# Kernel tuning notes

Measured on AMD Instinct MI355X. Metric: run time of the kernel, lower is better.

The kernel has to match this reference:

```python
import jax, jax.numpy as jnp
import numpy as np

TAU = 2.0
V_TH = 0.5
SG_ALPHA = 4.0
BN_EPS = 1e-5
NUM_HEADS = 8

@jax.custom_vjp
def spike_fn(x):
    return (x >= 0.0).astype(x.dtype)

def _spike_fwd(x):
    return (x >= 0.0).astype(x.dtype), x

def _spike_bwd(x, g):
    s = jax.nn.sigmoid(SG_ALPHA * x)
    return (g * SG_ALPHA * s * (1.0 - s),)

spike_fn.defvjp(_spike_fwd, _spike_bwd)

def lif(x_seq):
    """Multi-step LIF (spikingjelly step_mode='m'): x_seq [T, ...] -> spikes [T, ...].
    v <- v + (x - v)/tau ; spike = H(v - v_th) ; hard reset with detached spike."""
    def step(v, x):
        v = v + (x - v) / TAU
        s = spike_fn(v - V_TH)
        v = v * (1.0 - jax.lax.stop_gradient(s))
        return v, s
    _, s_seq = jax.lax.scan(step, jnp.zeros_like(x_seq[0]), x_seq)
    return s_seq

def conv1x1(x, w, b=None):
    # x: [T,B,C,H,W], w: [Cout,Cin]
    y = jnp.einsum('tbchw,oc->tbohw', x, w)
    if b is not None:
        y = y + b[:, None, None]
    return y

def bn(x, p):
    # eval-mode BatchNorm2d; p = [gamma, beta, mean, var] each [C]
    g, b, m, v = p[0], p[1], p[2], p[3]
    scale = g / jnp.sqrt(v + BN_EPS)
    return x * scale[:, None, None] + (b - m * scale)[:, None, None]

def setup_inputs() -> dict:
    key = jax.random.key(0)
    ks = jax.random.split(key, 20)
    T, B, C, H, W = 4, 8, 512, 32, 32
    Ch = 2048
    def bn_params(k, c):
        kk = jax.random.split(k, 4)
        gamma = jax.random.uniform(kk[0], (c,), jnp.float32, 0.5, 1.5)
        beta = jax.random.normal(kk[1], (c,), jnp.float32) * 0.1
        mean = jax.random.normal(kk[2], (c,), jnp.float32) * 0.1
        var = jax.random.uniform(kk[3], (c,), jnp.float32, 0.5, 1.5)
        return jnp.stack([gamma, beta, mean, var])
    s = 1.0 / np.sqrt(C)
    sh = 1.0 / np.sqrt(Ch)
    return {
        'x': jax.random.normal(ks[0], (T, B, C, H, W), jnp.float32),
        'q_w': jax.random.normal(ks[1], (C, C), jnp.float32) * s,
        'q_bn': bn_params(ks[2], C),
        'k_w': jax.random.normal(ks[3], (C, C), jnp.float32) * s,
        'k_bn': bn_params(ks[4], C),
        'v_w': jax.random.normal(ks[5], (C, C), jnp.float32) * s,
        'v_bn': bn_params(ks[6], C),
        'th_w': jax.random.normal(ks[7], (NUM_HEADS, NUM_HEADS), jnp.float32) / np.sqrt(NUM_HEADS),
        'proj_w': jax.random.normal(ks[8], (C, C), jnp.float32) * s,
        'proj_b': jax.random.normal(ks[9], (C,), jnp.float32) * 0.02,
        'proj_bn': bn_params(ks[10], C),
        'fc1_w': jax.random.normal(ks[11], (Ch, C), jnp.float32) * s,
        'fc1_b': jax.random.normal(ks[12], (Ch,), jnp.float32) * 0.02,
        'fc1_bn': bn_params(ks[13], Ch),
        'fc2_w': jax.random.normal(ks[14], (C, Ch), jnp.float32) * sh,
        'fc2_b': jax.random.normal(ks[15], (C,), jnp.float32) * 0.02,
        'fc2_bn': bn_params(ks[16], C),
    }

def reference(x, q_w, q_bn, k_w, k_bn, v_w, v_bn, th_w, proj_w, proj_b, proj_bn,
              fc1_w, fc1_b, fc1_bn, fc2_w, fc2_b, fc2_bn):
    T, B, C, H, W = x.shape
    N = H * W
    h = NUM_HEADS
    d = C // h

    # ---- MS_SSA_Conv ----
    identity = x
    xs = lif(x)  # shortcut_lif

    def to_heads(t):  # [T,B,C,H,W] -> [T,B,h,N,d]
        t = t.reshape(T, B, C, N).transpose(0, 1, 3, 2)        # [T,B,N,C]
        return t.reshape(T, B, N, h, d).transpose(0, 1, 3, 2, 4)

    q = to_heads(lif(bn(conv1x1(xs, q_w), q_bn)))
    k = to_heads(lif(bn(conv1x1(xs, k_w), k_bn)))
    v = to_heads(lif(bn(conv1x1(xs, v_w), v_bn)))

    kv = (k * v).sum(axis=3, keepdims=True)                    # [T,B,h,1,d]
    kv = jnp.einsum('tbhod,gh->tbgod', kv, th_w)               # talking heads (Conv1d k=1)
    kv = lif(kv)                                               # talking_heads_lif

    x_att = q * kv                                             # [T,B,h,N,d]
    x_att = x_att.transpose(0, 1, 2, 4, 3).reshape(T, B, C, H, W)
    x_out = bn(conv1x1(x_att, proj_w, proj_b), proj_bn) + identity

    # ---- MS_MLP_Conv (res=False since hidden != in) ----
    identity2 = x_out
    hdn = lif(bn(conv1x1(x_out, fc1_w, fc1_b), fc1_bn))
    out = lif(bn(conv1x1(hdn, fc2_w, fc2_b), fc2_bn)) + identity2
    return out
```

## Files before the change

### kernel.cpp

```cpp
#include <hip/hip_runtime.h>

typedef unsigned char u8;
typedef unsigned int u32;

#define T_STEPS 4
#define B_SZ 8
#define C_IN 512
#define CH 2048
#define N_SP 1024
#define S_C ((size_t)B_SZ * C_IN * N_SP)

__global__ __launch_bounds__(256) void lif_x_kernel(const float* __restrict__ in,
                                                    u8* __restrict__ out)
{
    size_t i = (size_t)blockIdx.x * 256 + threadIdx.x;
    float v = 0.0f;
    #pragma unroll
    for (int t = 0; t < T_STEPS; ++t) {
        float x = in[(size_t)t * S_C + i];
        v += (x - v) * 0.5f;
        u8 s = (v >= 0.5f) ? 1 : 0;
        out[(size_t)t * S_C + i] = s;
        v = s ? 0.0f : v;
    }
}

template<int MODE, int BSRC, bool BIAS, int K, int CO, int NSEL>
__global__ __launch_bounds__(256) void mm(
    const float* __restrict__ W0, const float* __restrict__ W1, const float* __restrict__ W2,
    const void* __restrict__ Xv,
    const float* __restrict__ bn0, const float* __restrict__ bn1, const float* __restrict__ bn2,
    const float* __restrict__ bias,
    const float* __restrict__ kvsf,
    const float* __restrict__ res,
    void* Y0, void* Y1, void* Y2)
{
    constexpr int BM = 64;
    constexpr int NB_CO = CO / BM;
    constexpr int KT = K / 16;

    __shared__ float As[16][72];
    __shared__ float Xs[16][136];

    const int bid = blockIdx.x;
    const int nblk = bid & 7;
    int slot = bid >> 3;
    const int cb = slot % NB_CO; slot /= NB_CO;
    const int sel = (NSEL > 1) ? (slot % NSEL) : 0;
    const int b   = (NSEL > 1) ? (slot / NSEL) : slot;

    const float* W   = (NSEL == 1 || sel == 0) ? W0  : (sel == 1 ? W1  : W2);
    const float* bnp = (NSEL == 1 || sel == 0) ? bn0 : (sel == 1 ? bn1 : bn2);
    void* Yv         = (NSEL == 1 || sel == 0) ? Y0  : (sel == 1 ? Y1  : Y2);

    const int coBase = cb * BM;
    const int n0blk = nblk * 128;
    const int tid = threadIdx.x;
    const int tx = tid & 15, ty = tid >> 4;

    const int wr = tid >> 2;
    const int wk4 = (tid & 3) * 4;

    float scale[4], shift[4];
    #pragma unroll
    for (int i = 0; i < 4; ++i) {
        const int co = coBase + ty * 4 + i;
        const float g = bnp[co], be = bnp[CO + co];
        const float mn = bnp[2 * CO + co], vr = bnp[3 * CO + co];
        scale[i] = g / sqrtf(vr + 1e-5f);
        shift[i] = be - mn * scale[i];
        if (BIAS) shift[i] += bias[co] * scale[i];
    }

    float vst[4][8];
    if (MODE != 1) {
        #pragma unroll
        for (int i = 0; i < 4; ++i)
            #pragma unroll
            for (int j = 0; j < 8; ++j) vst[i][j] = 0.0f;
    }

    for (int t = 0; t < T_STEPS; ++t) {
        const int tb = t * B_SZ + b;
        const u8* Xu = (const u8*)Xv + (size_t)tb * K * N_SP;
        const float* Xf = (const float*)Xv + (size_t)tb * K * N_SP;

        float acc[4][8];
        #pragma unroll
        for (int i = 0; i < 4; ++i)
            #pragma unroll
            for (int j = 0; j < 8; ++j) acc[i][j] = 0.0f;

        float4 wreg;
        u32 xa, xb;
        float mreg = 1.0f;
        float4 xfa, xfb;

        auto prefetch = [&](int kt) {
            wreg = *reinterpret_cast<const float4*>(
                W + (size_t)(coBase + wr) * K + kt * 16 + wk4);
            if constexpr (BSRC <= 1) {
                const u8* xp = Xu + (size_t)(kt * 16 + ty) * N_SP + n0blk + tx * 4;
                xa = *reinterpret_cast<const u32*>(xp);
                xb = *reinterpret_cast<const u32*>(xp + 64);
                if constexpr (BSRC == 1)
                    mreg = kvsf[(size_t)tb * K + kt * 16 + ty];
            } else {
                const float* xp = Xf + (size_t)(kt * 16 + ty) * N_SP + n0blk + tx * 4;
                xfa = *reinterpret_cast<const float4*>(xp);
                xfb = *reinterpret_cast<const float4*>(xp + 64);
            }
        };

        prefetch(0);

        for (int kt = 0; kt < KT; ++kt) {
            __syncthreads();
            As[wk4 + 0][wr] = wreg.x;
            As[wk4 + 1][wr] = wreg.y;
            As[wk4 + 2][wr] = wreg.z;
            As[wk4 + 3][wr] = wreg.w;
            if constexpr (BSRC <= 1) {
                float4 s0, s1;
                s0.x = (float)( xa        & 0xFFu);
                s0.y = (float)((xa >> 8 ) & 0xFFu);
                s0.z = (float)((xa >> 16) & 0xFFu);
                s0.w = (float)( xa >> 24        );
                s1.x = (float)( xb        & 0xFFu);
                s1.y = (float)((xb >> 8 ) & 0xFFu);
                s1.z = (float)((xb >> 16) & 0xFFu);
                s1.w = (float)( xb >> 24        );
                if constexpr (BSRC == 1) {
                    s0.x *= mreg; s0.y *= mreg; s0.z *= mreg; s0.w *= mreg;
                    s1.x *= mreg; s1.y *= mreg; s1.z *= mreg; s1.w *= mreg;
                }
                *reinterpret_cast<float4*>(&Xs[ty][tx * 4]) = s0;
                *reinterpret_cast<float4*>(&Xs[ty][tx * 4 + 64]) = s1;
            } else {
                *reinterpret_cast<float4*>(&Xs[ty][tx * 4]) = xfa;
                *reinterpret_cast<float4*>(&Xs[ty][tx * 4 + 64]) = xfb;
            }
            __syncthreads();
            if (kt + 1 < KT) prefetch(kt + 1);

            #pragma unroll
            for (int kk = 0; kk < 16; ++kk) {
                float4 av = *reinterpret_cast<const float4*>(&As[kk][ty * 4]);
                float4 x0 = *reinterpret_cast<const float4*>(&Xs[kk][tx * 4]);
                float4 x1 = *reinterpret_cast<const float4*>(&Xs[kk][tx * 4 + 64]);
                float wa[4] = {av.x, av.y, av.z, av.w};
                float xw[8] = {x0.x, x0.y, x0.z, x0.w, x1.x, x1.y, x1.z, x1.w};
                #pragma unroll
                for (int i = 0; i < 4; ++i)
                    #pragma unroll
                    for (int j = 0; j < 8; ++j)
                        acc[i][j] += wa[i] * xw[j];
            }
        }

        #pragma unroll
        for (int i = 0; i < 4; ++i) {
            const int co = coBase + ty * 4 + i;
            const size_t base = ((size_t)tb * CO + co) * N_SP + n0blk + tx * 4;
            if constexpr (MODE == 0) {
                u32 p0 = 0, p1 = 0;
                #pragma unroll
                for (int j = 0; j < 8; ++j) {
                    const float y = acc[i][j] * scale[i] + shift[i];
                    float v = vst[i][j];
                    v += (y - v) * 0.5f;
                    const u32 s = (v >= 0.5f) ? 1u : 0u;
                    vst[i][j] = s ? 0.0f : v;
                    if (j < 4) p0 |= s << (8 * j); else p1 |= s << (8 * (j - 4));
                }
                *reinterpret_cast<u32*>((u8*)Yv + base) = p0;
                *reinterpret_cast<u32*>((u8*)Yv + base + 64) = p1;
            } else if constexpr (MODE == 1) {
                float4 r0 = *reinterpret_cast<const float4*>(res + base);
                float4 r1 = *reinterpret_cast<const float4*>(res + base + 64);
                float rr[8] = {r0.x, r0.y, r0.z, r0.w, r1.x, r1.y, r1.z, r1.w};
                float o[8];
                #pragma unroll
                for (int j = 0; j < 8; ++j)
                    o[j] = acc[i][j] * scale[i] + shift[i] + rr[j];
                float4 s0 = {o[0], o[1], o[2], o[3]};
                float4 s1 = {o[4], o[5], o[6], o[7]};
                *reinterpret_cast<float4*>((float*)Yv + base) = s0;
                *reinterpret_cast<float4*>((float*)Yv + base + 64) = s1;
            } else {
                float* op = (float*)Yv + base;
                float4 r0 = *reinterpret_cast<const float4*>(op);
                float4 r1 = *reinterpret_cast<const float4*>(op + 64);
                float rr[8] = {r0.x, r0.y, r0.z, r0.w, r1.x, r1.y, r1.z, r1.w};
                float o[8];
                #pragma unroll
                for (int j = 0; j < 8; ++j) {
                    const float y = acc[i][j] * scale[i] + shift[i];
                    float v = vst[i][j];
                    v += (y - v) * 0.5f;
                    const u32 s = (v >= 0.5f) ? 1u : 0u;
                    vst[i][j] = s ? 0.0f : v;
                    o[j] = rr[j] + (s ? 1.0f : 0.0f);
                }
                float4 s0 = {o[0], o[1], o[2], o[3]};
                float4 s1 = {o[4], o[5], o[6], o[7]};
                *reinterpret_cast<float4*>(op) = s0;
                *reinterpret_cast<float4*>(op + 64) = s1;
            }
        }
    }
}

__global__ __launch_bounds__(256) void kv_reduce(const u8* __restrict__ ks,
                                                 const u8* __restrict__ vs,
                                                 float* __restrict__ kv)
{
    const int row = blockIdx.x * 4 + (threadIdx.x >> 6);
    const int lane = threadIdx.x & 63;
    const u8* kp = ks + (size_t)row * N_SP;
    const u8* vp = vs + (size_t)row * N_SP;
    int acc = 0;
    #pragma unroll
    for (int n = 0; n < N_SP; n += 256) {
        uchar4 a = *reinterpret_cast<const uchar4*>(kp + n + lane * 4);
        uchar4 c = *reinterpret_cast<const uchar4*>(vp + n + lane * 4);
        acc += (a.x & c.x) + (a.y & c.y) + (a.z & c.z) + (a.w & c.w);
    }
    #pragma unroll
    for (int off = 32; off; off >>= 1) acc += __shfl_down(acc, off, 64);
    if (lane == 0) kv[row] = (float)acc;
}

__global__ __launch_bounds__(256) void th_lif(const float* __restrict__ kvraw,
                                              const float* __restrict__ th,
                                              float* __restrict__ kvs)
{
    const int i = blockIdx.x * 256 + threadIdx.x;
    const int b = i >> 9;
    const int c = i & 511;
    const int g = c >> 6;
    const int dd = c & 63;
    float v = 0.0f;
    #pragma unroll
    for (int t = 0; t < T_STEPS; ++t) {
        const float* base = kvraw + ((size_t)t * B_SZ + b) * C_IN;
        float x = 0.0f;
        #pragma unroll
        for (int hh = 0; hh < 8; ++hh)
            x += base[hh * 64 + dd] * th[g * 8 + hh];
        v += (x - v) * 0.5f;
        const float s = (v >= 0.5f) ? 1.0f : 0.0f;
        kvs[((size_t)t * B_SZ + b) * C_IN + c] = s;
        v = (s != 0.0f) ? 0.0f : v;
    }
}

extern "C" void kernel_launch(void* const* d_in, const int* in_sizes, int n_in,
                              void* d_out, int out_size, void* d_ws, size_t ws_size,
                              hipStream_t stream)
{
    const float* x       = (const float*)d_in[0];
    const float* q_w     = (const float*)d_in[1];
    const float* q_bn    = (const float*)d_in[2];
    const float* k_w     = (const float*)d_in[3];
    const float* k_bn    = (const float*)d_in[4];
    const float* v_w     = (const float*)d_in[5];
    const float* v_bn    = (const float*)d_in[6];
    const float* th_w    = (const float*)d_in[7];
    const float* proj_w  = (const float*)d_in[8];
    const float* proj_b  = (const float*)d_in[9];
    const float* proj_bn = (const float*)d_in[10];
    const float* fc1_w   = (const float*)d_in[11];
    const float* fc1_b   = (const float*)d_in[12];
    const float* fc1_bn  = (const float*)d_in[13];
    const float* fc2_w   = (const float*)d_in[14];
    const float* fc2_b   = (const float*)d_in[15];
    const float* fc2_bn  = (const float*)d_in[16];
    float* out = (float*)d_out;

    u8* ws = (u8*)d_ws;
    const size_t SLOT = (size_t)T_STEPS * S_C;
    u8* xs = ws;
    u8* qs = ws + SLOT;
    u8* ks = ws + 2 * SLOT;
    u8* vs = ws + 3 * SLOT;
    float* kvraw = (float*)(ws + 4 * SLOT);
    float* kvsf  = kvraw + (size_t)T_STEPS * B_SZ * C_IN;
    u8* hdn = ws;

    lif_x_kernel<<<(int)(S_C / 256), 256, 0, stream>>>(x, xs);

    mm<0, 0, false, 512, 512, 3><<<1536, 256, 0, stream>>>(
        q_w, k_w, v_w, xs, q_bn, k_bn, v_bn, nullptr, nullptr, nullptr, qs, ks, vs);

    kv_reduce<<<(T_STEPS * B_SZ * C_IN) / 4, 256, 0, stream>>>(ks, vs, kvraw);
    th_lif<<<(B_SZ * C_IN) / 256, 256, 0, stream>>>(kvraw, th_w, kvsf);

    mm<1, 1, true, 512, 512, 1><<<512, 256, 0, stream>>>(
        proj_w, nullptr, nullptr, qs, proj_bn, nullptr, nullptr, proj_b, kvsf, x,
        out, nullptr, nullptr);

    mm<0, 2, true, 512, 2048, 1><<<2048, 256, 0, stream>>>(
        fc1_w, nullptr, nullptr, out, fc1_bn, nullptr, nullptr, fc1_b, nullptr, nullptr,
        hdn, nullptr, nullptr);

    mm<2, 0, true, 2048, 512, 1><<<512, 256, 0, stream>>>(
        fc2_w, nullptr, nullptr, hdn, fc2_bn, nullptr, nullptr, fc2_b, nullptr, nullptr,
        out, nullptr, nullptr);
}
```

Measured before the change: 2.641 ms.

## Double-buffer LDS tiles in the fused GEMM and prefetch across timesteps

Shared-memory tiles are now double-buffered, so each k-step needs one barrier instead of two. The next tile is staged into the alternate buffer after the compute, and prefetching carries across timestep boundaries so the pipeline does not drain at each t. This doubles LDS usage and changes the As row padding, which may affect occupancy and bank conflicts.

```diff
diff --git a/kernel.cpp b/kernel.cpp
--- a/kernel.cpp
+++ b/kernel.cpp
@@ -39,8 +39,8 @@
     constexpr int NB_CO = CO / BM;
     constexpr int KT = K / 16;
 
-    __shared__ float As[16][72];
-    __shared__ float Xs[16][136];
+    __shared__ float As[2][16][76];
+    __shared__ float Xs[2][16][136];
 
     const int bid = blockIdx.x;
     const int nblk = bid & 7;
@@ -80,10 +80,63 @@
             for (int j = 0; j < 8; ++j) vst[i][j] = 0.0f;
     }
 
+    float4 wreg;
+    u32 xa, xb;
+    float mreg = 1.0f;
+    float4 xfa, xfb;
+
+    auto prefetch = [&](int tbq, int kt) {
+        wreg = *reinterpret_cast<const float4*>(
+            W + (size_t)(coBase + wr) * K + kt * 16 + wk4);
+        if constexpr (BSRC <= 1) {
+            const u8* xp = (const u8*)Xv + (size_t)tbq * K * N_SP
+                           + (size_t)(kt * 16 + ty) * N_SP + n0blk + tx * 4;
+            xa = *reinterpret_cast<const u32*>(xp);
+            xb = *reinterpret_cast<const u32*>(xp + 64);
+            if constexpr (BSRC == 1)
+                mreg = kvsf[(size_t)tbq * K + kt * 16 + ty];
+        } else {
+            const float* xp = (const float*)Xv + (size_t)tbq * K * N_SP
+                              + (size_t)(kt * 16 + ty) * N_SP + n0blk + tx * 4;
+            xfa = *reinterpret_cast<const float4*>(xp);
+            xfb = *reinterpret_cast<const float4*>(xp + 64);
+        }
+    };
+
+    auto stage = [&](int pp) {
+        As[pp][wk4 + 0][wr] = wreg.x;
+        As[pp][wk4 + 1][wr] = wreg.y;
+        As[pp][wk4 + 2][wr] = wreg.z;
+        As[pp][wk4 + 3][wr] = wreg.w;
+        if constexpr (BSRC <= 1) {
+            float4 s0, s1;
+            s0.x = (float)( xa        & 0xFFu);
+            s0.y = (float)((xa >> 8 ) & 0xFFu);
+            s0.z = (float)((xa >> 16) & 0xFFu);
+            s0.w = (float)( xa >> 24        );
+            s1.x = (float)( xb        & 0xFFu);
+            s1.y = (float)((xb >> 8 ) & 0xFFu);
+            s1.z = (float)((xb >> 16) & 0xFFu);
+            s1.w = (float)( xb >> 24        );
+            if constexpr (BSRC == 1) {
+                s0.x *= mreg; s0.y *= mreg; s0.z *= mreg; s0.w *= mreg;
+                s1.x *= mreg; s1.y *= mreg; s1.z *= mreg; s1.w *= mreg;
+            }
+            *reinterpret_cast<float4*>(&Xs[pp][ty][tx * 4]) = s0;
+            *reinterpret_cast<float4*>(&Xs[pp][ty][tx * 4 + 64]) = s1;
+        } else {
+            *reinterpret_cast<float4*>(&Xs[pp][ty][tx * 4]) = xfa;
+            *reinterpret_cast<float4*>(&Xs[pp][ty][tx * 4 + 64]) = xfb;
+        }
+    };
+
+    int p = 0;
+    prefetch(b, 0);
+    stage(0);
+    __syncthreads();
+
     for (int t = 0; t < T_STEPS; ++t) {
         const int tb = t * B_SZ + b;
-        const u8* Xu = (const u8*)Xv + (size_t)tb * K * N_SP;
-        const float* Xf = (const float*)Xv + (size_t)tb * K * N_SP;
 
         float acc[4][8];
         #pragma unroll
@@ -91,63 +144,18 @@
             #pragma unroll
             for (int j = 0; j < 8; ++j) acc[i][j] = 0.0f;
 
-        float4 wreg;
-        u32 xa, xb;
-        float mreg = 1.0f;
-        float4 xfa, xfb;
-
-        auto prefetch = [&](int kt) {
-            wreg = *reinterpret_cast<const float4*>(
-                W + (size_t)(coBase + wr) * K + kt * 16 + wk4);
-            if constexpr (BSRC <= 1) {
-                const u8* xp = Xu + (size_t)(kt * 16 + ty) * N_SP + n0blk + tx * 4;
-                xa = *reinterpret_cast<const u32*>(xp);
-                xb = *reinterpret_cast<const u32*>(xp + 64);
-                if constexpr (BSRC == 1)
-                    mreg = kvsf[(size_t)tb * K + kt * 16 + ty];
-            } else {
-                const float* xp = Xf + (size_t)(kt * 16 + ty) * N_SP + n0blk + tx * 4;
-                xfa = *reinterpret_cast<const float4*>(xp);
-                xfb = *reinterpret_cast<const float4*>(xp + 64);
-            }
-        };
-
-        prefetch(0);
-
         for (int kt = 0; kt < KT; ++kt) {
-            __syncthreads();
-            As[wk4 + 0][wr] = wreg.x;
-            As[wk4 + 1][wr] = wreg.y;
-            As[wk4 + 2][wr] = wreg.z;
-            As[wk4 + 3][wr] = wreg.w;
-            if constexpr (BSRC <= 1) {
-                float4 s0, s1;
-                s0.x = (float)( xa        & 0xFFu);
-                s0.y = (float)((xa >> 8 ) & 0xFFu);
-                s0.z = (float)((xa >> 16) & 0xFFu);
-                s0.w = (float)( xa >> 24        );
-                s1.x = (float)( xb        & 0xFFu);
-                s1.y = (float)((xb >> 8 ) & 0xFFu);
-                s1.z = (float)((xb >> 16) & 0xFFu);
-                s1.w = (float)( xb >> 24        );
-                if constexpr (BSRC == 1) {
-                    s0.x *= mreg; s0.y *= mreg; s0.z *= mreg; s0.w *= mreg;
-                    s1.x *= mreg; s1.y *= mreg; s1.z *= mreg; s1.w *= mreg;
-                }
-                *reinterpret_cast<float4*>(&Xs[ty][tx * 4]) = s0;
-                *reinterpret_cast<float4*>(&Xs[ty][tx * 4 + 64]) = s1;
-            } else {
-                *reinterpret_cast<float4*>(&Xs[ty][tx * 4]) = xfa;
-                *reinterpret_cast<float4*>(&Xs[ty][tx * 4 + 64]) = xfb;
-            }
-            __syncthreads();
-            if (kt + 1 < KT) prefetch(kt + 1);
-
+            const bool last = (kt == KT - 1) && (t == T_STEPS - 1);
+            if (!last) {
+                const int nkt = (kt + 1 < KT) ? kt + 1 : 0;
+                const int ntb = (kt + 1 < KT) ? tb : tb + B_SZ;
+                prefetch(ntb, nkt);
+            }
             #pragma unroll
             for (int kk = 0; kk < 16; ++kk) {
-                float4 av = *reinterpret_cast<const float4*>(&As[kk][ty * 4]);
-                float4 x0 = *reinterpret_cast<const float4*>(&Xs[kk][tx * 4]);
-                float4 x1 = *reinterpret_cast<const float4*>(&Xs[kk][tx * 4 + 64]);
+                float4 av = *reinterpret_cast<const float4*>(&As[p][kk][ty * 4]);
+                float4 x0 = *reinterpret_cast<const float4*>(&Xs[p][kk][tx * 4]);
+                float4 x1 = *reinterpret_cast<const float4*>(&Xs[p][kk][tx * 4 + 64]);
                 float wa[4] = {av.x, av.y, av.z, av.w};
                 float xw[8] = {x0.x, x0.y, x0.z, x0.w, x1.x, x1.y, x1.z, x1.w};
                 #pragma unroll
@@ -155,6 +163,11 @@
                     #pragma unroll
                     for (int j = 0; j < 8; ++j)
                         acc[i][j] += wa[i] * xw[j];
+            }
+            if (!last) {
+                stage(p ^ 1);
+                __syncthreads();
+                p ^= 1;
             }
         }
 
```

New measurement: 4.356 ms. 1.65x slower.
